# Performance work log

Measured on AMD Instinct MI355X. Metric: run time of the kernel, lower is better.

## Reference

```python
import jax, jax.numpy as jnp
import numpy as np

D_MODEL = 1024
NUM_HEADS = 16
HEAD_DIM = D_MODEL // NUM_HEADS


def setup_inputs() -> dict:
    key = jax.random.key(0)
    ks = jax.random.split(key, 11)
    B, S = 2, 2048
    scale = 1.0 / np.sqrt(D_MODEL)
    inp = {
        "q": jax.random.normal(ks[0], (B, S, D_MODEL), jnp.float32),
        "k": jax.random.normal(ks[1], (B, S, D_MODEL), jnp.float32),
        "v": jax.random.normal(ks[2], (B, S, D_MODEL), jnp.float32),
        "Wq": jax.random.normal(ks[3], (D_MODEL, D_MODEL), jnp.float32) * scale,
        "bq": jnp.zeros((D_MODEL,), jnp.float32),
        "Wk": jax.random.normal(ks[4], (D_MODEL, D_MODEL), jnp.float32) * scale,
        "bk": jnp.zeros((D_MODEL,), jnp.float32),
        "Wv": jax.random.normal(ks[5], (D_MODEL, D_MODEL), jnp.float32) * scale,
        "bv": jnp.zeros((D_MODEL,), jnp.float32),
        "Wo": jax.random.normal(ks[6], (D_MODEL, D_MODEL), jnp.float32) * scale,
        "bo": jnp.zeros((D_MODEL,), jnp.float32),
    }
    return inp


def reference(q, k, v, Wq, bq, Wk, bk, Wv, bv, Wo, bo):
    B, S, _ = q.shape
    # Linear projections (torch Linear: x @ W.T + b), split into heads -> [b,h,s,d]
    def proj(x, W, b):
        y = jnp.einsum('bsm,nm->bsn', x, W) + b
        return y.reshape(B, -1, NUM_HEADS, HEAD_DIM).transpose(0, 2, 1, 3)
    qh = proj(q, Wq, bq)
    kh = proj(k, Wk, bk)
    vh = proj(v, Wv, bv)
    # NOTE: source scales by sqrt(d_model), NOT sqrt(head_dim) -- faithful quirk
    factor = jnp.sqrt(jnp.float32(D_MODEL))
    scores = jnp.einsum('bhqd,bhkd->bhqk', qh, kh) / factor
    attn = jax.nn.softmax(scores, axis=-1)
    out = jnp.einsum('bhqk,bhkd->bhqd', attn, vh)
    out = out.transpose(0, 2, 1, 3).reshape(B, S, D_MODEL)
    # out projection; dropout=0.0 (eval) is identity
    return jnp.einsum('bsm,nm->bsn', out, Wo) + bo
```

## Files before the change

kernel.cpp:

```cpp
#include <hip/hip_runtime.h>
#include <hip/hip_bf16.h>

typedef __hip_bfloat16 bf16;
typedef short short8 __attribute__((ext_vector_type(8)));
typedef float f32x4 __attribute__((ext_vector_type(4)));

#define MFMA_BF16(a, b, c) __builtin_amdgcn_mfma_f32_16x16x32_bf16(a, b, c, 0, 0, 0)

#define QSCALE 0.045084439f

__device__ __forceinline__ void async_copy16(const bf16* g, bf16* l) {
    __builtin_amdgcn_global_load_lds(
        (const __attribute__((address_space(1))) unsigned int*)(const void*)g,
        (__attribute__((address_space(3))) unsigned int*)(void*)l, 16, 0, 0);
}

__global__ __launch_bounds__(256) void convert_all(
    const float* __restrict__ q, const float* __restrict__ k, const float* __restrict__ v,
    const float* __restrict__ wq, const float* __restrict__ wk,
    const float* __restrict__ wv, const float* __restrict__ wo,
    bf16* __restrict__ qb, bf16* __restrict__ kb, bf16* __restrict__ vb,
    bf16* __restrict__ wqb, bf16* __restrict__ wkb, bf16* __restrict__ wvb,
    bf16* __restrict__ wob)
{
    int blk = blockIdx.x;
    const float* s; bf16* d; int rel;
    if      (blk < 1024) { s = q;  d = qb;  rel = blk; }
    else if (blk < 2048) { s = k;  d = kb;  rel = blk - 1024; }
    else if (blk < 3072) { s = v;  d = vb;  rel = blk - 2048; }
    else if (blk < 3328) { s = wq; d = wqb; rel = blk - 3072; }
    else if (blk < 3584) { s = wk; d = wkb; rel = blk - 3328; }
    else if (blk < 3840) { s = wv; d = wvb; rel = blk - 3584; }
    else                 { s = wo; d = wob; rel = blk - 3840; }
    size_t base = (size_t)rel * 1024 + threadIdx.x;
#pragma unroll
    for (int i = 0; i < 4; i++) {
        float4 f = ((const float4*)s)[base + i * 256];
        union { bf16 h[4]; uint2 u; } pk;
        pk.h[0] = (bf16)f.x; pk.h[1] = (bf16)f.y;
        pk.h[2] = (bf16)f.z; pk.h[3] = (bf16)f.w;
        ((uint2*)d)[base + i * 256] = pk.u;
    }
}

__global__ __launch_bounds__(256) void gemm_qkv(
    const bf16* __restrict__ qb, const bf16* __restrict__ kb, const bf16* __restrict__ vb,
    const bf16* __restrict__ wqb, const bf16* __restrict__ wkb, const bf16* __restrict__ wvb,
    const float* __restrict__ bq, const float* __restrict__ bk, const float* __restrict__ bv,
    bf16* __restrict__ Qp, bf16* __restrict__ Kp, bf16* __restrict__ Vt)
{
    __shared__ bf16 Al[128 * 64];
    __shared__ bf16 Bl[128 * 64];

    const int sel = blockIdx.x >> 3;
    const bf16* A; const bf16* W; const float* bias;
    if      (sel == 0) { A = qb; W = wqb; bias = bq; }
    else if (sel == 1) { A = kb; W = wkb; bias = bk; }
    else               { A = vb; W = wvb; bias = bv; }

    const int K = 1024, N = 1024;
    const int t = threadIdx.x;
    const int lane = t & 63, wave = t >> 6;
    const int ln = lane & 15, quad = lane >> 4;
    const int wm = wave >> 1, wn = wave & 1;
    const int m0 = blockIdx.y * 128, n0 = (blockIdx.x & 7) * 128;

    f32x4 acc[4][4];
#pragma unroll
    for (int i = 0; i < 4; i++)
#pragma unroll
        for (int j = 0; j < 4; j++) acc[i][j] = (f32x4){0.f, 0.f, 0.f, 0.f};

    const int lk = ln & 7;
    const int srow = t >> 3, sidx0 = t & 7;

    for (int k0 = 0; k0 < K; k0 += 64) {
        const bf16* Ab = A + (size_t)m0 * K + k0;
        const bf16* Wb = W + (size_t)n0 * K + k0;
#pragma unroll
        for (int p = 0; p < 4; p++) {
            int row = p * 32 + srow, idx = sidx0 ^ (row & 7);
            async_copy16(Ab + (size_t)row * K + idx * 8, &Al[(p * 256 + wave * 64) * 8]);
        }
#pragma unroll
        for (int p = 0; p < 4; p++) {
            int row = p * 32 + srow, idx = sidx0 ^ (row & 7);
            async_copy16(Wb + (size_t)row * K + idx * 8, &Bl[(p * 256 + wave * 64) * 8]);
        }
        __syncthreads();

#pragma unroll
        for (int kk = 0; kk < 2; kk++) {
            short8 af[4], bfr[4];
#pragma unroll
            for (int i = 0; i < 4; i++) {
                int r = wm * 64 + i * 16 + ln;
                af[i] = *(const short8*)&Al[r * 64 + (((kk << 2) | quad) ^ lk) * 8];
            }
#pragma unroll
            for (int j = 0; j < 4; j++) {
                int r = wn * 64 + j * 16 + ln;
                bfr[j] = *(const short8*)&Bl[r * 64 + (((kk << 2) | quad) ^ lk) * 8];
            }
#pragma unroll
            for (int i = 0; i < 4; i++)
#pragma unroll
                for (int j = 0; j < 4; j++)
                    acc[i][j] = MFMA_BF16(af[i], bfr[j], acc[i][j]);
        }
        __syncthreads();
    }

#pragma unroll
    for (int j = 0; j < 4; j++) {
        int c = n0 + wn * 64 + j * 16 + ln;
        float bv2 = bias[c];
        if (sel == 2) {
            int h = c >> 6, dd = c & 63;
#pragma unroll
            for (int i = 0; i < 4; i++) {
                int m = m0 + wm * 64 + i * 16 + quad * 4;
                int bb = m >> 11, s = m & 2047;
                union { bf16 h4[4]; uint2 u; } pk;
#pragma unroll
                for (int r = 0; r < 4; r++) pk.h4[r] = (bf16)(acc[i][j][r] + bv2);
                *(uint2*)&Vt[(((size_t)(bb * 16 + h)) * 64 + dd) * 2048 + s] = pk.u;
            }
        } else {
            bf16* out = (sel == 0) ? Qp : Kp;
            float scl = (sel == 0) ? QSCALE : 1.0f;
#pragma unroll
            for (int i = 0; i < 4; i++) {
                int rb = m0 + wm * 64 + i * 16 + quad * 4;
#pragma unroll
                for (int r = 0; r < 4; r++)
                    out[(size_t)(rb + r) * N + c] = (bf16)((acc[i][j][r] + bv2) * scl);
            }
        }
    }
}

__global__ __launch_bounds__(256) void gemm_fin(
    const bf16* __restrict__ A, const bf16* __restrict__ W,
    const float* __restrict__ bias, float* __restrict__ C)
{
    __shared__ bf16 Al[128 * 64];
    __shared__ bf16 Bl[64 * 64];

    const int K = 1024, N = 1024;
    const int t = threadIdx.x;
    const int lane = t & 63, wave = t >> 6;
    const int ln = lane & 15, quad = lane >> 4;
    const int wm = wave >> 1, wn = wave & 1;
    const int m0 = blockIdx.y * 128, n0 = blockIdx.x * 64;

    f32x4 acc[4][2];
#pragma unroll
    for (int i = 0; i < 4; i++)
#pragma unroll
        for (int j = 0; j < 2; j++) acc[i][j] = (f32x4){0.f, 0.f, 0.f, 0.f};

    const int lk = ln & 7;
    const int srow = t >> 3, sidx0 = t & 7;

    for (int k0 = 0; k0 < K; k0 += 64) {
        const bf16* Ab = A + (size_t)m0 * K + k0;
        const bf16* Wb = W + (size_t)n0 * K + k0;
#pragma unroll
        for (int p = 0; p < 4; p++) {
            int row = p * 32 + srow, idx = sidx0 ^ (row & 7);
            async_copy16(Ab + (size_t)row * K + idx * 8, &Al[(p * 256 + wave * 64) * 8]);
        }
#pragma unroll
        for (int p = 0; p < 2; p++) {
            int row = p * 32 + srow, idx = sidx0 ^ (row & 7);
            async_copy16(Wb + (size_t)row * K + idx * 8, &Bl[(p * 256 + wave * 64) * 8]);
        }
        __syncthreads();

#pragma unroll
        for (int kk = 0; kk < 2; kk++) {
            short8 af[4], bfr[2];
#pragma unroll
            for (int i = 0; i < 4; i++) {
                int r = wm * 64 + i * 16 + ln;
                af[i] = *(const short8*)&Al[r * 64 + (((kk << 2) | quad) ^ lk) * 8];
            }
#pragma unroll
            for (int j = 0; j < 2; j++) {
                int r = wn * 32 + j * 16 + ln;
                bfr[j] = *(const short8*)&Bl[r * 64 + (((kk << 2) | quad) ^ lk) * 8];
            }
#pragma unroll
            for (int i = 0; i < 4; i++)
#pragma unroll
                for (int j = 0; j < 2; j++)
                    acc[i][j] = MFMA_BF16(af[i], bfr[j], acc[i][j]);
        }
        __syncthreads();
    }

#pragma unroll
    for (int j = 0; j < 2; j++) {
        int c = n0 + wn * 32 + j * 16 + ln;
        float bv2 = bias[c];
#pragma unroll
        for (int i = 0; i < 4; i++) {
            int rb = m0 + wm * 64 + i * 16 + quad * 4;
#pragma unroll
            for (int r = 0; r < 4; r++)
                C[(size_t)(rb + r) * N + c] = acc[i][j][r] + bv2;
        }
    }
}

__global__ __launch_bounds__(256) void attn128q(
    const bf16* __restrict__ Q, const bf16* __restrict__ K,
    const bf16* __restrict__ V, bf16* __restrict__ O)
{
    const int S = 2048, D = 1024, LDP = 136;
    __shared__ bf16 Kl[128 * 64];
    __shared__ bf16 Vl[64 * 128];
    __shared__ bf16 Pl[4][16 * LDP];

    const int t = threadIdx.x, lane = t & 63, wave = t >> 6;
    const int ln = lane & 15, quad = lane >> 4;
    const int qt = blockIdx.x, h = blockIdx.y, b = blockIdx.z;
    const size_t kqbase = (size_t)b * S * D + (size_t)h * 64;
    const size_t vbase = ((size_t)(b * 16 + h)) * 64 * 2048;

    short8 aq[2][2];
#pragma unroll
    for (int g = 0; g < 2; g++) {
        const bf16* qp = Q + kqbase + (size_t)(qt * 128 + g * 64 + wave * 16 + ln) * D;
        aq[g][0] = *(const short8*)(qp + quad * 8);
        aq[g][1] = *(const short8*)(qp + 32 + quad * 8);
    }

    f32x4 o[2][4];
    float l[2][4];
#pragma unroll
    for (int g = 0; g < 2; g++)
#pragma unroll
        for (int i = 0; i < 4; i++) { o[g][i] = (f32x4){0.f, 0.f, 0.f, 0.f}; l[g][i] = 0.f; }

    const int lk = ln & 7;
    const int kof0 = ln * 64 + ((quad ^ lk) * 8);
    const int kof1 = ln * 64 + (((4 | quad) ^ lk) * 8);
    int vof[4];
#pragma unroll
    for (int kk = 0; kk < 4; kk++) vof[kk] = ln * 128 + ((((kk << 2) | quad) ^ lk) * 8);
    const int pwb = (quad * 4) * LDP + ln;
    const int prb = ln * LDP + quad * 8;
    bf16* pw = &Pl[wave][0];

    const int krow = t >> 3, kidx = t & 7;
    const int vrow = t >> 4, vidx = t & 15;

    for (int kt = 0; kt < S / 128; kt++) {
#pragma unroll
        for (int p = 0; p < 4; p++) {
            int row = p * 32 + krow, idx = kidx ^ (row & 7);
            async_copy16(K + kqbase + (size_t)(kt * 128 + row) * D + idx * 8,
                         &Kl[(p * 256 + wave * 64) * 8]);
        }
#pragma unroll
        for (int p = 0; p < 4; p++) {
            int row = p * 16 + vrow, idx = vidx ^ (row & 7);
            async_copy16(V + vbase + (size_t)row * 2048 + kt * 128 + idx * 8,
                         &Vl[(p * 256 + wave * 64) * 8]);
        }
        __syncthreads();

#pragma unroll
        for (int g = 0; g < 2; g++) {
            f32x4 s[8];
#pragma unroll
            for (int nk = 0; nk < 8; nk++) {
                short8 b0 = *(const short8*)&Kl[kof0 + nk * 1024];
                short8 b1 = *(const short8*)&Kl[kof1 + nk * 1024];
                f32x4 a = (f32x4){0.f, 0.f, 0.f, 0.f};
                a = MFMA_BF16(aq[g][0], b0, a);
                a = MFMA_BF16(aq[g][1], b1, a);
                s[nk] = a;
            }
#pragma unroll
            for (int nk = 0; nk < 8; nk++)
#pragma unroll
                for (int r = 0; r < 4; r++) {
                    float p = __builtin_amdgcn_exp2f(s[nk][r]);
                    l[g][r] += p;
                    pw[pwb + r * LDP + nk * 16] = (bf16)p;
                }
            short8 pa[4];
#pragma unroll
            for (int kk = 0; kk < 4; kk++)
                pa[kk] = *(const short8*)&pw[prb + kk * 32];
#pragma unroll
            for (int nd = 0; nd < 4; nd++)
#pragma unroll
                for (int kk = 0; kk < 4; kk++) {
                    short8 vb = *(const short8*)&Vl[nd * 2048 + vof[kk]];
                    o[g][nd] = MFMA_BF16(pa[kk], vb, o[g][nd]);
                }
        }
        __syncthreads();
    }

#pragma unroll
    for (int g = 0; g < 2; g++)
#pragma unroll
        for (int r = 0; r < 4; r++) {
            float v = l[g][r];
            v += __shfl_xor(v, 1);
            v += __shfl_xor(v, 2);
            v += __shfl_xor(v, 4);
            v += __shfl_xor(v, 8);
            float inv = __builtin_amdgcn_rcpf(v);
#pragma unroll
            for (int nd = 0; nd < 4; nd++) {
                int row = qt * 128 + g * 64 + wave * 16 + quad * 4 + r;
                O[((size_t)b * S + row) * D + h * 64 + nd * 16 + ln] =
                    (bf16)(o[g][nd][r] * inv);
            }
        }
}

extern "C" void kernel_launch(void* const* d_in, const int* in_sizes, int n_in,
                              void* d_out, int out_size, void* d_ws, size_t ws_size,
                              hipStream_t stream) {
    (void)in_sizes; (void)n_in; (void)out_size; (void)ws_size;
    const float* q  = (const float*)d_in[0];
    const float* k  = (const float*)d_in[1];
    const float* v  = (const float*)d_in[2];
    const float* Wq = (const float*)d_in[3];
    const float* bq = (const float*)d_in[4];
    const float* Wk = (const float*)d_in[5];
    const float* bk = (const float*)d_in[6];
    const float* Wv = (const float*)d_in[7];
    const float* bv = (const float*)d_in[8];
    const float* Wo = (const float*)d_in[9];
    const float* bo = (const float*)d_in[10];
    float* out = (float*)d_out;

    const int M = 4096, N = 1024;
    const size_t MN = (size_t)M * N;
    const size_t NN = (size_t)N * N;
    bf16* qb  = (bf16*)d_ws;
    bf16* kb  = qb + MN;
    bf16* vb  = kb + MN;
    bf16* wqb = vb + MN;
    bf16* wkb = wqb + NN;
    bf16* wvb = wkb + NN;
    bf16* wob = wvb + NN;
    bf16* Qp  = wob + NN;
    bf16* Kp  = Qp + MN;
    bf16* Vt  = Kp + MN;
    bf16* AO  = qb;

    dim3 blk(256);
    convert_all<<<4096, blk, 0, stream>>>(q, k, v, Wq, Wk, Wv, Wo,
                                          qb, kb, vb, wqb, wkb, wvb, wob);

    gemm_qkv<<<dim3(24, 32), blk, 0, stream>>>(qb, kb, vb, wqb, wkb, wvb,
                                               bq, bk, bv, Qp, Kp, Vt);

    attn128q<<<dim3(16, 16, 2), blk, 0, stream>>>(Qp, Kp, Vt, AO);

    gemm_fin<<<dim3(16, 32), blk, 0, stream>>>(AO, wob, bo, out);
}
```

Measured before the change: 244.5 us.

## Compute transposed scores so P stays in registers for PV MFMA

The QK^T MFMA operands are swapped so each lane holds scores in the layout that the 16x16x16 bf16 MFMA expects for its A operand. The probabilities can then feed the PV product straight from registers, which removes the per-wave LDS staging buffer for P along with its write/read round trip. The PV product now uses the smaller K=16 MFMA with 4-element V loads, so it issues twice as many MFMA instructions. The row-sum reduction is changed to shuffle across quads to match the transposed layout.

```diff
diff --git a/kernel.cpp b/kernel.cpp
--- a/kernel.cpp
+++ b/kernel.cpp
@@ -3,9 +3,11 @@
 
 typedef __hip_bfloat16 bf16;
 typedef short short8 __attribute__((ext_vector_type(8)));
+typedef short bs4 __attribute__((ext_vector_type(4)));
 typedef float f32x4 __attribute__((ext_vector_type(4)));
 
 #define MFMA_BF16(a, b, c) __builtin_amdgcn_mfma_f32_16x16x32_bf16(a, b, c, 0, 0, 0)
+#define MFMA16_BF16(a, b, c) __builtin_amdgcn_mfma_f32_16x16x16bf16_1k(a, b, c, 0, 0, 0)
 
 #define QSCALE 0.045084439f
 
@@ -218,10 +220,9 @@
     const bf16* __restrict__ Q, const bf16* __restrict__ K,
     const bf16* __restrict__ V, bf16* __restrict__ O)
 {
-    const int S = 2048, D = 1024, LDP = 136;
+    const int S = 2048, D = 1024;
     __shared__ bf16 Kl[128 * 64];
     __shared__ bf16 Vl[64 * 128];
-    __shared__ bf16 Pl[4][16 * LDP];
 
     const int t = threadIdx.x, lane = t & 63, wave = t >> 6;
     const int ln = lane & 15, quad = lane >> 4;
@@ -238,21 +239,19 @@
     }
 
     f32x4 o[2][4];
-    float l[2][4];
+    float l[2] = {0.f, 0.f};
 #pragma unroll
     for (int g = 0; g < 2; g++)
 #pragma unroll
-        for (int i = 0; i < 4; i++) { o[g][i] = (f32x4){0.f, 0.f, 0.f, 0.f}; l[g][i] = 0.f; }
+        for (int i = 0; i < 4; i++) o[g][i] = (f32x4){0.f, 0.f, 0.f, 0.f};
 
     const int lk = ln & 7;
     const int kof0 = ln * 64 + ((quad ^ lk) * 8);
     const int kof1 = ln * 64 + (((4 | quad) ^ lk) * 8);
-    int vof[4];
-#pragma unroll
-    for (int kk = 0; kk < 4; kk++) vof[kk] = ln * 128 + ((((kk << 2) | quad) ^ lk) * 8);
-    const int pwb = (quad * 4) * LDP + ln;
-    const int prb = ln * LDP + quad * 8;
-    bf16* pw = &Pl[wave][0];
+    int vof[8];
+#pragma unroll
+    for (int nk = 0; nk < 8; nk++)
+        vof[nk] = ln * 128 + (((nk * 2 + (quad >> 1)) ^ lk) * 8 + (quad & 1) * 4);
 
     const int krow = t >> 3, kidx = t & 7;
     const int vrow = t >> 4, vidx = t & 15;
@@ -273,57 +272,49 @@
         __syncthreads();
 
 #pragma unroll
-        for (int g = 0; g < 2; g++) {
-            f32x4 s[8];
-#pragma unroll
-            for (int nk = 0; nk < 8; nk++) {
-                short8 b0 = *(const short8*)&Kl[kof0 + nk * 1024];
-                short8 b1 = *(const short8*)&Kl[kof1 + nk * 1024];
+        for (int nk = 0; nk < 8; nk++) {
+            short8 kf0 = *(const short8*)&Kl[nk * 1024 + kof0];
+            short8 kf1 = *(const short8*)&Kl[nk * 1024 + kof1];
+            bs4 pa[2];
+#pragma unroll
+            for (int g = 0; g < 2; g++) {
                 f32x4 a = (f32x4){0.f, 0.f, 0.f, 0.f};
-                a = MFMA_BF16(aq[g][0], b0, a);
-                a = MFMA_BF16(aq[g][1], b1, a);
-                s[nk] = a;
-            }
-#pragma unroll
-            for (int nk = 0; nk < 8; nk++)
+                a = MFMA_BF16(kf0, aq[g][0], a);
+                a = MFMA_BF16(kf1, aq[g][1], a);
+                union { bs4 s4; bf16 hh[4]; } pk;
 #pragma unroll
                 for (int r = 0; r < 4; r++) {
-                    float p = __builtin_amdgcn_exp2f(s[nk][r]);
-                    l[g][r] += p;
-                    pw[pwb + r * LDP + nk * 16] = (bf16)p;
+                    float p = __builtin_amdgcn_exp2f(a[r]);
+                    l[g] += p;
+                    pk.hh[r] = (bf16)p;
                 }
-            short8 pa[4];
-#pragma unroll
-            for (int kk = 0; kk < 4; kk++)
-                pa[kk] = *(const short8*)&pw[prb + kk * 32];
+                pa[g] = pk.s4;
+            }
+#pragma unroll
+            for (int nd = 0; nd < 4; nd++) {
+                bs4 vb = *(const bs4*)&Vl[nd * 2048 + vof[nk]];
+                o[0][nd] = MFMA16_BF16(pa[0], vb, o[0][nd]);
+                o[1][nd] = MFMA16_BF16(pa[1], vb, o[1][nd]);
+            }
+        }
+        __syncthreads();
+    }
+
+#pragma unroll
+    for (int g = 0; g < 2; g++) {
+        float lv = l[g];
+        lv += __shfl_xor(lv, 16);
+        lv += __shfl_xor(lv, 32);
+#pragma unroll
+        for (int r = 0; r < 4; r++) {
+            float inv = __builtin_amdgcn_rcpf(__shfl(lv, quad * 4 + r));
+            int row = qt * 128 + g * 64 + wave * 16 + quad * 4 + r;
 #pragma unroll
             for (int nd = 0; nd < 4; nd++)
-#pragma unroll
-                for (int kk = 0; kk < 4; kk++) {
-                    short8 vb = *(const short8*)&Vl[nd * 2048 + vof[kk]];
-                    o[g][nd] = MFMA_BF16(pa[kk], vb, o[g][nd]);
-                }
-        }
-        __syncthreads();
-    }
-
-#pragma unroll
-    for (int g = 0; g < 2; g++)
-#pragma unroll
-        for (int r = 0; r < 4; r++) {
-            float v = l[g][r];
-            v += __shfl_xor(v, 1);
-            v += __shfl_xor(v, 2);
-            v += __shfl_xor(v, 4);
-            v += __shfl_xor(v, 8);
-            float inv = __builtin_amdgcn_rcpf(v);
-#pragma unroll
-            for (int nd = 0; nd < 4; nd++) {
-                int row = qt * 128 + g * 64 + wave * 16 + quad * 4 + r;
                 O[((size_t)b * S + row) * D + h * 64 + nd * 16 + ln] =
                     (bf16)(o[g][nd][r] * inv);
-            }
-        }
+        }
+    }
 }
 
 extern "C" void kernel_launch(void* const* d_in, const int* in_sizes, int n_in,
```

Measured after the change: 229.8 us. 1.06x faster.
